# Optimization experiments

Hardware: AMD Instinct MI355X
Metric: run time of the kernel (lower is better)

The kernel has to match this reference:

```python
import jax, jax.numpy as jnp
import numpy as np

B, N, C = 16, 1024, 768            # N = window_size**2 = 32*32
NUM_HEADS, BANK = 12, 256
HEAD_DIM = C // NUM_HEADS
LN_EPS = 1e-5


def setup_inputs() -> dict:
    key = jax.random.key(0)
    ks = jax.random.split(key, 9)
    s = 0.02
    return {
        "x": jax.random.normal(ks[0], (B, N, C), dtype=jnp.float32),
        "qkv_w": jax.random.normal(ks[1], (3 * C, C), dtype=jnp.float32) * s,
        "qkv_b": jnp.zeros((3 * C,), dtype=jnp.float32),
        "proj_w": jax.random.normal(ks[2], (C, C), dtype=jnp.float32) * s,
        "proj_b": jnp.zeros((C,), dtype=jnp.float32),
        "norm_w": jnp.ones((C,), dtype=jnp.float32),
        "norm_b": jnp.zeros((C,), dtype=jnp.float32),
        "bank_k": jax.random.normal(ks[3], (BANK, C), dtype=jnp.float32) * s,
        "bank_v": jax.random.normal(ks[4], (BANK, C), dtype=jnp.float32) * s,
    }


def _split_heads_bank(bank, b):
    # (BANK, C) -> broadcast to (b, BANK, C) -> (b, H, BANK, D)
    t = jnp.broadcast_to(bank, (b,) + bank.shape)
    return t.reshape(b, BANK, NUM_HEADS, HEAD_DIM).transpose(0, 2, 1, 3)


def reference(x, qkv_w, qkv_b, proj_w, proj_b, norm_w, norm_b, bank_k, bank_v):
    b, n, c = x.shape
    h, d = NUM_HEADS, HEAD_DIM
    # QKV projection: (b, n, 3c) -> (3, b, h, n, d)
    qkv = (jnp.einsum("bnc,fc->bnf", x, qkv_w) + qkv_b)
    qkv = qkv.reshape(b, n, 3, h, d).transpose(2, 0, 3, 1, 4)
    q, k, v = qkv[0], qkv[1], qkv[2]
    # Memory-bank read + concat onto KV
    k_full = jnp.concatenate([k, _split_heads_bank(bank_k, b)], axis=2)  # (b,h,n+BANK,d)
    v_full = jnp.concatenate([v, _split_heads_bank(bank_v, b)], axis=2)
    # SDPA (dropout_p = 0.0)
    scores = jnp.einsum("bhnd,bhmd->bhnm", q, k_full) / jnp.sqrt(jnp.asarray(d, x.dtype))
    attn = jax.nn.softmax(scores, axis=-1)
    out = jnp.einsum("bhnm,bhmd->bhnd", attn, v_full)
    out = out.transpose(0, 2, 1, 3).reshape(b, n, c)
    # Bank write value: LayerNorm(proj(out))  (side effect in torch; returned here)
    p = jnp.einsum("bnc,oc->bno", out, proj_w) + proj_b
    mu = jnp.mean(p, axis=-1, keepdims=True)
    var = jnp.mean(jnp.square(p - mu), axis=-1, keepdims=True)
    bank_update = (p - mu) * jax.lax.rsqrt(var + LN_EPS) * norm_w + norm_b
    return out, bank_update
```

## Files before the change

### kernel.cpp

```cpp
#include <hip/hip_runtime.h>

typedef __attribute__((ext_vector_type(8))) short short8;
typedef __attribute__((ext_vector_type(4))) float float4_t;
typedef unsigned short u16;

#define K_DIM 768

__device__ __forceinline__ u16 f2bf(float f) {
  union { float f; unsigned u; } v; v.f = f;
  unsigned r = v.u + 0x7FFFu + ((v.u >> 16) & 1u);
  return (u16)(r >> 16);
}

__device__ __forceinline__ u16 f2bf_trunc(float f) {
  union { float f; unsigned u; } v; v.f = f;
  return (u16)(v.u >> 16);
}

__device__ __forceinline__ void gload16(const void* g, void* l) {
  __builtin_amdgcn_global_load_lds(
      (__attribute__((address_space(1))) void*)g,
      (__attribute__((address_space(3))) void*)l, 16, 0, 0);
}

__global__ __launch_bounds__(256) void cvt_all_kernel(
    const float* __restrict__ x, const float* __restrict__ qw,
    const float* __restrict__ pw, const float* __restrict__ bkf,
    const float* __restrict__ bvf,
    u16* __restrict__ xbf, u16* __restrict__ qwbf, u16* __restrict__ pwbf,
    u16* __restrict__ bk, u16* __restrict__ bvt) {
  const int blk = blockIdx.x;
  if (blk < 14592) {
    int i = blk * 256 + threadIdx.x;
    const float* src; u16* dst;
    if (i < 3145728)      { src = x;  dst = xbf; }
    else if (i < 3588096) { src = qw; dst = qwbf; i -= 3145728; }
    else                  { src = pw; dst = pwbf; i -= 3588096; }
    float4 v = ((const float4*)src)[i];
    union { u16 h[4]; unsigned long long ll; } o;
    o.h[0] = f2bf(v.x); o.h[1] = f2bf(v.y); o.h[2] = f2bf(v.z); o.h[3] = f2bf(v.w);
    ((unsigned long long*)dst)[i] = o.ll;
  } else {
    int idx = (blk - 14592) * 256 + threadIdx.x;
    int m = idx / 768;
    int c = idx - m * 768;
    int h = c >> 6, d = c & 63;
    bk[(h * 256 + m) * 64 + d] = f2bf(bkf[idx]);
    bvt[(h * 64 + d) * 256 + m] = f2bf(bvf[idx]);
  }
}


#define SBAR()                                 \
  do {                                         \
    __builtin_amdgcn_sched_barrier(0);         \
    __builtin_amdgcn_s_barrier();              \
    __builtin_amdgcn_sched_barrier(0);         \
  } while (0)

#define VMW2()                                                  \
  do {                                                          \
    __builtin_amdgcn_sched_barrier(0);                          \
    asm volatile("s_waitcnt vmcnt(2)" ::: "memory");            \
  } while (0)

#define VMW0()                                                  \
  do {                                                          \
    __builtin_amdgcn_sched_barrier(0);                          \
    asm volatile("s_waitcnt vmcnt(0)" ::: "memory");            \
  } while (0)

#define LDA(B_, MH)                                                            \
  _Pragma("unroll") for (int m_ = 0; m_ < 4; m_++) {                           \
    const char* p_ =                                                           \
        (const char*)As[B_] + ((wm * 128 + (MH) * 64 + m_ * 16) << 7);         \
    af[m_][0] = *(const short8*)(p_ + ab0);                                    \
    af[m_][1] = *(const short8*)(p_ + ab1);                                    \
  }

#define LDB(B_, NH, BF)                                                        \
  _Pragma("unroll") for (int n_ = 0; n_ < 2; n_++) {                           \
    const char* p_ =                                                           \
        (const char*)Bs[B_] + ((wn * 64 + (NH) * 32 + n_ * 16) << 7);          \
    BF[n_][0] = *(const short8*)(p_ + ab0);                                    \
    BF[n_][1] = *(const short8*)(p_ + ab1);                                    \
  }

#define MFMAQ(MH, NH, BF)                                                      \
  do {                                                                         \
    __builtin_amdgcn_s_setprio(1);                                             \
    _Pragma("unroll") for (int m_ = 0; m_ < 4; m_++)                           \
        _Pragma("unroll") for (int n_ = 0; n_ < 2; n_++) {                     \
      acc[(MH) * 4 + m_][(NH) * 2 + n_] =                                      \
          __builtin_amdgcn_mfma_f32_16x16x32_bf16(                             \
              af[m_][0], BF[n_][0], acc[(MH) * 4 + m_][(NH) * 2 + n_], 0, 0,   \
              0);                                                              \
      acc[(MH) * 4 + m_][(NH) * 2 + n_] =                                      \
          __builtin_amdgcn_mfma_f32_16x16x32_bf16(                             \
              af[m_][1], BF[n_][1], acc[(MH) * 4 + m_][(NH) * 2 + n_], 0, 0,   \
              0);                                                              \
    }                                                                          \
    __builtin_amdgcn_s_setprio(0);                                             \
  } while (0)

template <int MODE>
__global__ __launch_bounds__(512, 2) void gemm256(
    const u16* __restrict__ A, const u16* __restrict__ Bw,
    const float* __restrict__ bias,
    u16* __restrict__ q_ws, u16* __restrict__ k_ws, u16* __restrict__ vt_ws,
    float* __restrict__ p_out) {
  __shared__ u16 As[2][16384];
  __shared__ u16 Bs[2][16384];
  const int tid = threadIdx.x;
  const int w = tid >> 6, lane = tid & 63;
  const int l15 = lane & 15, quad = lane >> 4;
  const int wm = w >> 2, wn = w & 3;

  constexpr int NBN = (MODE == 0) ? 9 : 3;
  const int bid = blockIdx.x;
  const int xcd = bid & 7, local = bid >> 3;
  const int bm = xcd * 8 + local / NBN;
  const int bn = local % NBN;

  int soff[2], loff[2];
#pragma unroll
  for (int r = 0; r < 2; r++) {
    const int off = r * 8192 + tid * 16;
    const int row = off >> 7;
    const int grp = (off & 127) >> 4;
    soff[r] = row * K_DIM + ((grp ^ (row & 7)) * 8);
    loff[r] = off;
  }
  const u16* Abase = A + (size_t)bm * 256 * K_DIM;
  const u16* Bbase = Bw + (size_t)bn * 256 * K_DIM;

  auto stg = [&](const u16* g0, u16* l0) {
    gload16(g0 + soff[0], (char*)l0 + loff[0]);
    gload16(g0 + soff[1], (char*)l0 + loff[1]);
  };

  const int ab0 = l15 * 128 + (((0 * 4 + quad) ^ (l15 & 7)) << 4);
  const int ab1 = l15 * 128 + (((1 * 4 + quad) ^ (l15 & 7)) << 4);

  float4_t acc[8][4];
#pragma unroll
  for (int i = 0; i < 8; i++)
#pragma unroll
    for (int j = 0; j < 4; j++) acc[i][j] = (float4_t){0.f, 0.f, 0.f, 0.f};

  short8 af[4][2], bf0[2][2], bf1[2][2];

  stg(Abase, &As[0][0]);
  stg(Abase + 128 * K_DIM, &As[0][8192]);
  stg(Bbase, &Bs[0][0]);
  stg(Bbase + 128 * K_DIM, &Bs[0][8192]);
  stg(Abase + 64, &As[1][0]);
  VMW2();
  SBAR();

#pragma unroll 1
  for (int g = 0; g < 5; g++) {
    const int kt_o = g * 128 + 64;
    const int kt_p = g * 128 + 128;
    const int kt_q = g * 128 + 192;
    LDA(0, 0); LDB(0, 0, bf0);
    stg(Abase + 128 * K_DIM + kt_o, &As[1][8192]);
    SBAR(); MFMAQ(0, 0, bf0); SBAR();
    LDB(0, 1, bf1);
    stg(Bbase + kt_o, &Bs[1][0]);
    SBAR(); MFMAQ(0, 1, bf1); SBAR();
    LDA(0, 1);
    stg(Bbase + 128 * K_DIM + kt_o, &Bs[1][8192]);
    SBAR(); MFMAQ(1, 1, bf1); SBAR();
    stg(Abase + kt_p, &As[0][0]);
    VMW2(); SBAR(); MFMAQ(1, 0, bf0); SBAR();
    LDA(1, 0); LDB(1, 0, bf0);
    stg(Abase + 128 * K_DIM + kt_p, &As[0][8192]);
    SBAR(); MFMAQ(0, 0, bf0); SBAR();
    LDB(1, 1, bf1);
    stg(Bbase + kt_p, &Bs[0][0]);
    SBAR(); MFMAQ(0, 1, bf1); SBAR();
    LDA(1, 1);
    stg(Bbase + 128 * K_DIM + kt_p, &Bs[0][8192]);
    SBAR(); MFMAQ(1, 1, bf1); SBAR();
    stg(Abase + kt_q, &As[1][0]);
    VMW2(); SBAR(); MFMAQ(1, 0, bf0); SBAR();
  }

  {
    const int kt_o = 704;
    LDA(0, 0); LDB(0, 0, bf0);
    stg(Abase + 128 * K_DIM + kt_o, &As[1][8192]);
    SBAR(); MFMAQ(0, 0, bf0); SBAR();
    LDB(0, 1, bf1);
    stg(Bbase + kt_o, &Bs[1][0]);
    SBAR(); MFMAQ(0, 1, bf1); SBAR();
    LDA(0, 1);
    stg(Bbase + 128 * K_DIM + kt_o, &Bs[1][8192]);
    SBAR(); MFMAQ(1, 1, bf1); SBAR();
    VMW0(); SBAR(); MFMAQ(1, 0, bf0); SBAR();
    LDA(1, 0); LDB(1, 0, bf0);
    SBAR(); MFMAQ(0, 0, bf0); SBAR();
    LDB(1, 1, bf1);
    SBAR(); MFMAQ(0, 1, bf1); SBAR();
    LDA(1, 1);
    SBAR(); MFMAQ(1, 1, bf1); SBAR();
    MFMAQ(1, 0, bf0);
  }

  const float QS = 0.18033688011112042f;
#pragma unroll
  for (int mi = 0; mi < 8; mi++) {
#pragma unroll
    for (int ni = 0; ni < 4; ni++) {
      const int row0 = bm * 256 + wm * 128 + mi * 16 + quad * 4;
      const int f = bn * 256 + wn * 64 + ni * 16 + l15;
      const float bv = bias[f];
      if (MODE == 0) {
        const int which = f / 768;
        const int rem = f - which * 768;
        const int h = rem >> 6, d = rem & 63;
#pragma unroll
        for (int r2 = 0; r2 < 4; r2++) {
          float v = acc[mi][ni][r2] + bv;
          const int i = row0 + r2;
          const int bb = i >> 10, n = i & 1023;
          const size_t bhh = (size_t)(bb * 12 + h);
          if (which == 0)      q_ws[(bhh * 1024 + n) * 64 + d] = f2bf(v * QS);
          else if (which == 1) k_ws[(bhh * 1024 + n) * 64 + d] = f2bf(v);
          else                 vt_ws[(bhh * 64 + d) * 1024 + n] = f2bf(v);
        }
      } else {
#pragma unroll
        for (int r2 = 0; r2 < 4; r2++) {
          const int i = row0 + r2;
          p_out[(size_t)i * 768 + f] = acc[mi][ni][r2] + bv;
        }
      }
    }
  }
}

__global__ __launch_bounds__(256) void fa_kernel(
    const u16* __restrict__ qws, const u16* __restrict__ kws,
    const u16* __restrict__ vtws, const u16* __restrict__ bk,
    const u16* __restrict__ bvt,
    float* __restrict__ out, u16* __restrict__ obf) {
  __shared__ u16 smem[8192];
  u16* Ks  = smem;
  u16* Vts = smem + 4096;

  const int tid = threadIdx.x;
  const int w = tid >> 6, lane = tid & 63;
  const int l15 = lane & 15, quad = lane >> 4;
  u16* Psw = smem + w * 2048;
  const int bh = blockIdx.x;
  const int b = bh / 12, h = bh - b * 12;
  const int q0 = blockIdx.y * 128 + w * 32;

  short8 qf[2][2];
  {
    const u16* qb = qws + ((size_t)bh * 1024 + q0) * 64;
#pragma unroll
    for (int rt = 0; rt < 2; rt++)
#pragma unroll
      for (int c = 0; c < 2; c++)
        qf[rt][c] = *(const short8*)(qb + (rt * 16 + l15) * 64 + c * 32 + quad * 8);
  }

  const short ONE = (short)0x3F80;
  const short8 onesf = (short8){ONE, ONE, ONE, ONE, ONE, ONE, ONE, ONE};

  float4_t O[2][4];
  float4_t lacc[2];
#pragma unroll
  for (int rt = 0; rt < 2; rt++) {
#pragma unroll
    for (int dt = 0; dt < 4; dt++) O[rt][dt] = (float4_t){0.f, 0.f, 0.f, 0.f};
    lacc[rt] = (float4_t){0.f, 0.f, 0.f, 0.f};
  }

  for (int t = 0; t < 20; t++) {
    const int mb = t * 64;
    __syncthreads();
#pragma unroll
    for (int r = 0; r < 2; r++) {
      const int off = (w * 2 + r) * 1024 + lane * 16;
      const int row = off >> 7;
      const int grp = (off & 127) >> 4;
      const int lcol = (grp ^ (row & 7)) * 8;
      const u16* g = (mb < 1024)
          ? kws + ((size_t)bh * 1024 + mb + row) * 64 + lcol
          : bk + ((size_t)h * 256 + (mb - 1024) + row) * 64 + lcol;
      gload16(g, (char*)Ks + off);
      const u16* g2 = (mb < 1024)
          ? vtws + ((size_t)bh * 64 + row) * 1024 + mb + lcol
          : bvt + ((size_t)h * 64 + row) * 256 + (mb - 1024) + lcol;
      gload16(g2, (char*)Vts + off);
    }
    __syncthreads();

    short8 kf[4][2];
#pragma unroll
    for (int ct = 0; ct < 4; ct++)
#pragma unroll
      for (int c = 0; c < 2; c++) {
        const int row = ct * 16 + l15;
        kf[ct][c] = *(const short8*)(Ks + row * 64 + ((c * 4 + quad) ^ (row & 7)) * 8);
      }

    float4_t S[2][4];
#pragma unroll
    for (int rt = 0; rt < 2; rt++)
#pragma unroll
      for (int ct = 0; ct < 4; ct++) {
        float4_t z = (float4_t){0.f, 0.f, 0.f, 0.f};
        z = __builtin_amdgcn_mfma_f32_16x16x32_bf16(qf[rt][0], kf[ct][0], z, 0, 0, 0);
        S[rt][ct] = __builtin_amdgcn_mfma_f32_16x16x32_bf16(qf[rt][1], kf[ct][1], z, 0, 0, 0);
      }

    short8 vf[4][2];
#pragma unroll
    for (int dt = 0; dt < 4; dt++)
#pragma unroll
      for (int c = 0; c < 2; c++) {
        const int row = dt * 16 + l15;
        vf[dt][c] = *(const short8*)(Vts + row * 64 + ((c * 4 + quad) ^ (row & 7)) * 8);
      }

    __syncthreads();

#pragma unroll
    for (int rt = 0; rt < 2; rt++) {
#pragma unroll
      for (int ct = 0; ct < 4; ct++) {
        const int colg = ct * 2 + (l15 >> 3);
#pragma unroll
        for (int r = 0; r < 4; r++) {
          const float p = __builtin_amdgcn_exp2f(S[rt][ct][r]);
          const int q = rt * 16 + quad * 4 + r;
          Psw[q * 64 + (colg ^ (q & 7)) * 8 + (l15 & 7)] = f2bf_trunc(p);
        }
      }
    }

#pragma unroll
    for (int rt = 0; rt < 2; rt++)
#pragma unroll
      for (int c = 0; c < 2; c++) {
        const int qrow = rt * 16 + l15;
        const short8 pf = *(const short8*)(&Psw[qrow * 64 + (((c * 4 + quad) ^ (qrow & 7)) * 8)]);
#pragma unroll
        for (int dt = 0; dt < 4; dt++)
          O[rt][dt] = __builtin_amdgcn_mfma_f32_16x16x32_bf16(pf, vf[dt][c], O[rt][dt], 0, 0, 0);
        lacc[rt] = __builtin_amdgcn_mfma_f32_16x16x32_bf16(pf, onesf, lacc[rt], 0, 0, 0);
      }
  }

#pragma unroll
  for (int rt = 0; rt < 2; rt++) {
    float rl[4];
#pragma unroll
    for (int r = 0; r < 4; r++) rl[r] = 1.f / lacc[rt][r];
#pragma unroll
    for (int dt = 0; dt < 4; dt++)
#pragma unroll
      for (int r = 0; r < 4; r++) {
        const float v = O[rt][dt][r] * rl[r];
        const int n = q0 + rt * 16 + quad * 4 + r;
        const int d = dt * 16 + l15;
        const size_t idx = ((size_t)b * 1024 + n) * 768 + h * 64 + d;
        out[idx] = v;
        obf[idx] = f2bf(v);
      }
  }
}

__global__ __launch_bounds__(256) void ln_kernel(float* __restrict__ p,
                                                 const float* __restrict__ nw,
                                                 const float* __restrict__ nb) {
  __shared__ float red[2][4];
  const int row = blockIdx.x, tid = threadIdx.x;
  float* pr = p + (size_t)row * 768;
  const float x0 = pr[tid], x1 = pr[tid + 256], x2 = pr[tid + 512];
  float s = x0 + x1 + x2;
  float sq = x0 * x0 + x1 * x1 + x2 * x2;
#pragma unroll
  for (int m = 1; m < 64; m <<= 1) {
    s += __shfl_xor(s, m, 64);
    sq += __shfl_xor(sq, m, 64);
  }
  const int w = tid >> 6;
  if ((tid & 63) == 0) { red[0][w] = s; red[1][w] = sq; }
  __syncthreads();
  s = red[0][0] + red[0][1] + red[0][2] + red[0][3];
  sq = red[1][0] + red[1][1] + red[1][2] + red[1][3];
  const float mean = s * (1.0f / 768.0f);
  const float var = sq * (1.0f / 768.0f) - mean * mean;
  const float rstd = rsqrtf(var + 1e-5f);
  pr[tid]       = (x0 - mean) * rstd * nw[tid]       + nb[tid];
  pr[tid + 256] = (x1 - mean) * rstd * nw[tid + 256] + nb[tid + 256];
  pr[tid + 512] = (x2 - mean) * rstd * nw[tid + 512] + nb[tid + 512];
}

extern "C" void kernel_launch(void* const* d_in, const int* in_sizes, int n_in,
                              void* d_out, int out_size, void* d_ws, size_t ws_size,
                              hipStream_t stream) {
  (void)in_sizes; (void)n_in; (void)out_size; (void)ws_size;
  const float* x      = (const float*)d_in[0];
  const float* qkv_w  = (const float*)d_in[1];
  const float* qkv_b  = (const float*)d_in[2];
  const float* proj_w = (const float*)d_in[3];
  const float* proj_b = (const float*)d_in[4];
  const float* norm_w = (const float*)d_in[5];
  const float* norm_b = (const float*)d_in[6];
  const float* bank_k = (const float*)d_in[7];
  const float* bank_v = (const float*)d_in[8];

  char* ws = (char*)d_ws;
  u16* xbf   = (u16*)(ws + 0);
  u16* obf   = (u16*)(ws + 0);
  u16* qwbf  = (u16*)(ws + 25165824);
  u16* pwbf  = (u16*)(ws + 28704768);
  u16* bkbf  = (u16*)(ws + 29884416);
  u16* bvtbf = (u16*)(ws + 30277632);
  u16* q_ws  = (u16*)(ws + 30670848);
  u16* k_ws  = (u16*)(ws + 55836672);
  u16* vt_ws = (u16*)(ws + 81002496);

  float* out0  = (float*)d_out;
  float* p_out = out0 + 12582912;

  cvt_all_kernel<<<15360, 256, 0, stream>>>(x, qkv_w, proj_w, bank_k, bank_v,
                                            xbf, qwbf, pwbf, bkbf, bvtbf);

  gemm256<0><<<dim3(576), 512, 0, stream>>>(xbf, qwbf, qkv_b, q_ws, k_ws, vt_ws, nullptr);
  fa_kernel<<<dim3(192, 8), 256, 0, stream>>>(q_ws, k_ws, vt_ws, bkbf, bvtbf, out0, obf);
  gemm256<1><<<dim3(192), 512, 0, stream>>>(obf, pwbf, proj_b, nullptr, nullptr, nullptr, p_out);
  ln_kernel<<<16384, 256, 0, stream>>>(p_out, norm_w, norm_b);
}
```

Measured before the change: 425.7 us.

## Double-buffer K/V tiles in flash-attention kernel with prefetch of next tile

Splits shared memory into two K/V buffers and issues the global-to-LDS loads for the next tile before computing on the current one. The aim is to hide global load latency behind the MFMA and softmax work. Block-wide syncs are replaced with explicit waitcnt plus s_barrier and sched_barrier fences, and launch bounds now request 4 blocks per CU. The cost is doubled LDS use per block, which may limit occupancy. The P scratch area now aliases the current buffer, which depends on the fence ordering being correct.

Result: slower. 699.4 us (+64.3%).

```diff
diff --git a/kernel.cpp b/kernel.cpp
--- a/kernel.cpp
+++ b/kernel.cpp
@@ -241,19 +241,16 @@
   }
 }
 
-__global__ __launch_bounds__(256) void fa_kernel(
+__global__ __launch_bounds__(256, 4) void fa_kernel(
     const u16* __restrict__ qws, const u16* __restrict__ kws,
     const u16* __restrict__ vtws, const u16* __restrict__ bk,
     const u16* __restrict__ bvt,
     float* __restrict__ out, u16* __restrict__ obf) {
-  __shared__ u16 smem[8192];
-  u16* Ks  = smem;
-  u16* Vts = smem + 4096;
+  __shared__ u16 smem[2][8192];
 
   const int tid = threadIdx.x;
   const int w = tid >> 6, lane = tid & 63;
   const int l15 = lane & 15, quad = lane >> 4;
-  u16* Psw = smem + w * 2048;
   const int bh = blockIdx.x;
   const int b = bh / 12, h = bh - b * 12;
   const int q0 = blockIdx.y * 128 + w * 32;
@@ -280,9 +277,10 @@
     lacc[rt] = (float4_t){0.f, 0.f, 0.f, 0.f};
   }
 
-  for (int t = 0; t < 20; t++) {
-    const int mb = t * 64;
-    __syncthreads();
+  auto stage = [&](int tt, int buf) {
+    const int mb = tt * 64;
+    u16* Ksb = &smem[buf][0];
+    u16* Vtb = &smem[buf][4096];
 #pragma unroll
     for (int r = 0; r < 2; r++) {
       const int off = (w * 2 + r) * 1024 + lane * 16;
@@ -292,13 +290,28 @@
       const u16* g = (mb < 1024)
           ? kws + ((size_t)bh * 1024 + mb + row) * 64 + lcol
           : bk + ((size_t)h * 256 + (mb - 1024) + row) * 64 + lcol;
-      gload16(g, (char*)Ks + off);
+      gload16(g, (char*)Ksb + off);
       const u16* g2 = (mb < 1024)
           ? vtws + ((size_t)bh * 64 + row) * 1024 + mb + lcol
           : bvt + ((size_t)h * 64 + row) * 256 + (mb - 1024) + lcol;
-      gload16(g2, (char*)Vts + off);
+      gload16(g2, (char*)Vtb + off);
     }
-    __syncthreads();
+  };
+
+  stage(0, 0);
+  __builtin_amdgcn_sched_barrier(0);
+  asm volatile("s_waitcnt vmcnt(0)" ::: "memory");
+  __builtin_amdgcn_s_barrier();
+  __builtin_amdgcn_sched_barrier(0);
+
+#pragma unroll 1
+  for (int t = 0; t < 20; t++) {
+    const int cur = t & 1;
+    if (t < 19) stage(t + 1, cur ^ 1);
+
+    const u16* Ks  = &smem[cur][0];
+    const u16* Vts = &smem[cur][4096];
+    u16* Psw = &smem[cur][0] + w * 2048;
 
     short8 kf[4][2];
 #pragma unroll
@@ -328,7 +341,10 @@
         vf[dt][c] = *(const short8*)(Vts + row * 64 + ((c * 4 + quad) ^ (row & 7)) * 8);
       }
 
-    __syncthreads();
+    __builtin_amdgcn_sched_barrier(0);
+    asm volatile("s_waitcnt lgkmcnt(0)" ::: "memory");
+    __builtin_amdgcn_s_barrier();
+    __builtin_amdgcn_sched_barrier(0);
 
 #pragma unroll
     for (int rt = 0; rt < 2; rt++) {
@@ -355,6 +371,11 @@
           O[rt][dt] = __builtin_amdgcn_mfma_f32_16x16x32_bf16(pf, vf[dt][c], O[rt][dt], 0, 0, 0);
         lacc[rt] = __builtin_amdgcn_mfma_f32_16x16x32_bf16(pf, onesf, lacc[rt], 0, 0, 0);
       }
+
+    __builtin_amdgcn_sched_barrier(0);
+    asm volatile("s_waitcnt vmcnt(0) lgkmcnt(0)" ::: "memory");
+    __builtin_amdgcn_s_barrier();
+    __builtin_amdgcn_sched_barrier(0);
   }
 
 #pragma unroll
```
